# Performance work log

Measured on AMD Instinct MI355X. Metric: run time of the kernel, lower is better.

## Reference

```python
import jax, jax.numpy as jnp
import numpy as np

LEVELS = 16
FEATURES = 2
HASHMAP_SIZE = 524288  # 2**19
BASE_RES = 16
PER_LEVEL_SCALE = 1.5
N_POINTS = 2097152  # 2**21

# Per-level grid resolutions, computed exactly like the torch code: int(base*scale**l)
_RES = np.array([int(BASE_RES * PER_LEVEL_SCALE ** l) for l in range(LEVELS)], dtype=np.float32)

# Instant-NGP spatial hash primes
_P1, _P2, _P3 = np.int32(73856093), np.int32(19349663), np.int32(83492791)


def setup_inputs() -> dict:
    key = jax.random.key(0)
    k1, k2 = jax.random.split(key)
    x = jax.random.uniform(k1, (N_POINTS, 3), dtype=jnp.float32)
    # Stacked learned hash tables: [L, T, F], init randn*0.01 as in the module
    tables = jax.random.normal(k2, (LEVELS, HASHMAP_SIZE, FEATURES), dtype=jnp.float32) * 0.01
    return {"x": x, "tables": tables}


def reference(x, tables):
    # x: [N, 3] float; tables: [L, T, F] float
    res = jnp.asarray(_RES)                       # [L]
    pos = x[None, :, :] * res[:, None, None]      # [L, N, 3]
    p = jnp.floor(pos).astype(jnp.int32)          # [L, N, 3] (matches torch .int())
    # Spatial hash with int32 wrap-around, identical to torch int32 semantics
    h = (p[..., 0] * _P1) ^ (p[..., 1] * _P2) ^ (p[..., 2] * _P3)
    idx = jnp.mod(h, np.int32(HASHMAP_SIZE))      # [L, N], nonnegative (sign of divisor)
    emb = jax.vmap(lambda t, i: t[i])(tables, idx)  # [L, N, F] per-level gather
    n = x.shape[0]
    # concat over levels along last dim -> [N, L*F]
    return jnp.transpose(emb, (1, 0, 2)).reshape(n, LEVELS * FEATURES)
```

## Files before the change

### kernel.cpp

```cpp
#include <hip/hip_runtime.h>

#define LEVELS 16
#define TSIZE 524288
#define TMASK (TSIZE - 1)
#define TPB 256
#define GPPT 8
#define CHUNK (TPB * GPPT)

typedef float f2v __attribute__((ext_vector_type(2)));
typedef float f4v __attribute__((ext_vector_type(4)));

__device__ __constant__ float c_res[LEVELS] = {
    16.f, 24.f, 36.f, 54.f, 81.f, 121.f, 182.f, 273.f,
    410.f, 615.f, 922.f, 1383.f, 2075.f, 3113.f, 4670.f, 7006.f
};

__device__ __forceinline__ unsigned hash_idx(float px, float py, float pz, float r)
{
    const int ix = (int)floorf(px * r);
    const int iy = (int)floorf(py * r);
    const int iz = (int)floorf(pz * r);
    const unsigned h = (unsigned)ix * 73856093u
                     ^ (unsigned)iy * 19349663u
                     ^ (unsigned)iz * 83492791u;
    return h & TMASK;
}



__global__ __launch_bounds__(TPB) void hash_kernel(
    const float* __restrict__ x,
    unsigned* __restrict__ idxw,
    int n)
{
    __shared__ float xs[CHUNK * 3];
    const int c = blockIdx.x;
    const int t = threadIdx.x;
    const long long base = (long long)c * CHUNK;
    unsigned* __restrict__ islab = idxw + (size_t)c * LEVELS * CHUNK;

    if (base + CHUNK <= n) {
        const f4v* __restrict__ xg = reinterpret_cast<const f4v*>(x + 3 * base);
#pragma unroll
        for (int j = 0; j < 6; ++j) {
            const int s = j * TPB + t;
            *reinterpret_cast<f4v*>(&xs[4 * s]) = xg[s];
        }
        __syncthreads();

#pragma unroll
        for (int j = 0; j < GPPT; ++j) {
            const int local = j * TPB + t;
            const float px = xs[3 * local + 0];
            const float py = xs[3 * local + 1];
            const float pz = xs[3 * local + 2];
#pragma unroll
            for (int l = 0; l < LEVELS; ++l)
                islab[l * CHUNK + local] = hash_idx(px, py, pz, c_res[l]);
        }
    } else {
        for (int j = 0; j < GPPT; ++j) {
            const int local = j * TPB + t;
            const long long p = base + local;
            if (p < n) {
                const float px = x[3 * p + 0];
                const float py = x[3 * p + 1];
                const float pz = x[3 * p + 2];
                for (int l = 0; l < LEVELS; ++l)
                    islab[l * CHUNK + local] = hash_idx(px, py, pz, c_res[l]);
            }
        }
    }
}

__global__ __launch_bounds__(TPB) void gather_kernel(
    const unsigned* __restrict__ idxr,
    const float* __restrict__ tables,
    f2v* __restrict__ ws,
    int n, int bpl)
{
    const int b = blockIdx.x;
    const int half = b / (8 * bpl);
    const int r = b % (8 * bpl);
    const int level = half * 8 + (r & 7);
    const int c = r >> 3;
    const int t = threadIdx.x;

    const float* __restrict__ tbl = tables + (size_t)level * (TSIZE * 2);
    f2v* __restrict__ slab = ws + ((size_t)c * LEVELS + level) * CHUNK;
    const unsigned* __restrict__ islab = idxr + ((size_t)c * LEVELS + level) * CHUNK;
    const long long base = (long long)c * CHUNK;

    if (base + CHUNK <= n) {
        unsigned idx[GPPT];
#pragma unroll
        for (int j = 0; j < GPPT; ++j)
            idx[j] = islab[j * TPB + t];

        f2v e[GPPT];
#pragma unroll
        for (int j = 0; j < GPPT; ++j)
            e[j] = *reinterpret_cast<const f2v*>(tbl + 2 * (size_t)idx[j]);

#pragma unroll
        for (int j = 0; j < GPPT; ++j)
            __builtin_nontemporal_store(e[j], slab + j * TPB + t);
    } else {
        for (int j = 0; j < GPPT; ++j) {
            const int local = j * TPB + t;
            if (base + local < n) {
                const unsigned id = islab[local];
                const f2v e = *reinterpret_cast<const f2v*>(tbl + 2 * (size_t)id);
                __builtin_nontemporal_store(e, slab + local);
            }
        }
    }
}

__global__ __launch_bounds__(TPB) void gather_x_kernel(
    const float* __restrict__ x,
    const float* __restrict__ tables,
    f2v* __restrict__ ws,
    int n, int bpl)
{
    const int b = blockIdx.x;
    const int half = b / (8 * bpl);
    const int r = b % (8 * bpl);
    const int level = half * 8 + (r & 7);
    const int c = r >> 3;
    const int t = threadIdx.x;

    const float rs = c_res[level];
    const float* __restrict__ tbl = tables + (size_t)level * (TSIZE * 2);
    f2v* __restrict__ slab = ws + ((size_t)c * LEVELS + level) * CHUNK;
    const long long base = (long long)c * CHUNK;

    if (base + CHUNK <= n) {
        const float* __restrict__ xb = x + 3 * base;
        float px[GPPT], py[GPPT], pz[GPPT];
#pragma unroll
        for (int j = 0; j < GPPT; ++j) {
            const int local = j * TPB + t;
            px[j] = xb[3 * local + 0];
            py[j] = xb[3 * local + 1];
            pz[j] = xb[3 * local + 2];
        }
        unsigned idx[GPPT];
#pragma unroll
        for (int j = 0; j < GPPT; ++j)
            idx[j] = hash_idx(px[j], py[j], pz[j], rs);
        f2v e[GPPT];
#pragma unroll
        for (int j = 0; j < GPPT; ++j)
            e[j] = *reinterpret_cast<const f2v*>(tbl + 2 * (size_t)idx[j]);
#pragma unroll
        for (int j = 0; j < GPPT; ++j)
            __builtin_nontemporal_store(e[j], slab + j * TPB + t);
    } else {
#pragma unroll
        for (int j = 0; j < GPPT; ++j) {
            const int local = j * TPB + t;
            const long long p = base + local;
            if (p < n) {
                const float qx = x[3 * p + 0];
                const float qy = x[3 * p + 1];
                const float qz = x[3 * p + 2];
                const unsigned idx = hash_idx(qx, qy, qz, rs);
                const f2v e = *reinterpret_cast<const f2v*>(tbl + 2 * (size_t)idx);
                __builtin_nontemporal_store(e, slab + local);
            }
        }
    }
}

__global__ __launch_bounds__(TPB) void assemble_kernel(
    const f2v* __restrict__ ws,
    float* __restrict__ out,
    int n)
{
    const int c = blockIdx.x;
    const int t = threadIdx.x;
    const int q = t & 7;
    const int sub = t >> 3;

    const f2v* __restrict__ wa = ws + ((size_t)c * LEVELS + 2 * q) * CHUNK;
    const f2v* __restrict__ wb = wa + CHUNK;
    const long long base = (long long)c * CHUNK;

    if (base + CHUNK <= n) {
#pragma unroll 8
        for (int u = 0; u < CHUNK / 64; ++u) {
            const int lp = 2 * (u * 32 + sub);
            const f4v a = __builtin_nontemporal_load(
                reinterpret_cast<const f4v*>(wa + lp));
            const f4v b = __builtin_nontemporal_load(
                reinterpret_cast<const f4v*>(wb + lp));
            f4v v0, v1;
            v0.x = a.x; v0.y = a.y; v0.z = b.x; v0.w = b.y;
            v1.x = a.z; v1.y = a.w; v1.z = b.z; v1.w = b.w;
            float* row = out + (size_t)(base + lp) * (2 * LEVELS) + 4 * q;
            __builtin_nontemporal_store(v0, reinterpret_cast<f4v*>(row));
            __builtin_nontemporal_store(v1, reinterpret_cast<f4v*>(row + 2 * LEVELS));
        }
    } else {
#pragma unroll 8
        for (int u = 0; u < CHUNK / 32; ++u) {
            const int lp = u * 32 + sub;
            const long long pt = base + lp;
            if (pt < n) {
                const f2v a = __builtin_nontemporal_load(wa + lp);
                const f2v b = __builtin_nontemporal_load(wb + lp);
                f4v v;
                v.x = a.x; v.y = a.y; v.z = b.x; v.w = b.y;
                __builtin_nontemporal_store(
                    v, reinterpret_cast<f4v*>(out + (size_t)pt * (2 * LEVELS) + 4 * q));
            }
        }
    }
}

#define ROWW 34
__global__ __launch_bounds__(TPB) void hashgrid_fused(
    const float* __restrict__ x,
    const float* __restrict__ tables,
    float* __restrict__ out,
    int n)
{
    __shared__ float lds[TPB * ROWW];
    const int t = threadIdx.x;

    for (long long base = (long long)blockIdx.x * TPB; base < n;
         base += (long long)gridDim.x * TPB) {
        const int p = (int)base + t;
        float px = 0.f, py = 0.f, pz = 0.f;
        if (p < n) {
            px = x[3 * (size_t)p + 0];
            py = x[3 * (size_t)p + 1];
            pz = x[3 * (size_t)p + 2];
        }
#pragma unroll
        for (int l = 0; l < LEVELS; ++l) {
            if (p < n) {
                const unsigned idx = hash_idx(px, py, pz, c_res[l]);
                const f2v e = *reinterpret_cast<const f2v*>(
                    tables + (((size_t)l * TSIZE + idx) << 1));
                *reinterpret_cast<f2v*>(lds + t * ROWW + 2 * l) = e;
            }
            __syncthreads();
        }
#pragma unroll
        for (int it = 0; it < 8; ++it) {
            const int lp = it * 32 + (t >> 3);
            const int qq = t & 7;
            const int gp = (int)base + lp;
            if (gp < n) {
                const f2v a = *reinterpret_cast<const f2v*>(lds + lp * ROWW + 4 * qq);
                const f2v b = *reinterpret_cast<const f2v*>(lds + lp * ROWW + 4 * qq + 2);
                f4v v;
                v.x = a.x; v.y = a.y; v.z = b.x; v.w = b.y;
                __builtin_nontemporal_store(
                    v, reinterpret_cast<f4v*>(out + (size_t)gp * (2 * LEVELS) + 4 * qq));
            }
        }
        __syncthreads();
    }
}

extern "C" void kernel_launch(void* const* d_in, const int* in_sizes, int n_in,
                              void* d_out, int out_size, void* d_ws, size_t ws_size,
                              hipStream_t stream)
{
    const float* x      = (const float*)d_in[0];
    const float* tables = (const float*)d_in[1];
    float* out          = (float*)d_out;
    const int n = in_sizes[0] / 3;

    const int bpl = (n + CHUNK - 1) / CHUNK;
    const size_t slab_bytes = (size_t)bpl * LEVELS * CHUNK * sizeof(f2v);
    const size_t idx_bytes  = (size_t)bpl * LEVELS * CHUNK * sizeof(unsigned);

    if (ws_size < slab_bytes) {
        int grid = 1024;
        const int nblocks = (n + TPB - 1) / TPB;
        if (nblocks < grid) grid = nblocks;
        hashgrid_fused<<<grid, TPB, 0, stream>>>(x, tables, out, n);
        return;
    }

    f2v* ws = (f2v*)d_ws;

    if (ws_size >= slab_bytes + idx_bytes) {
        unsigned* idxw = (unsigned*)((char*)d_ws + slab_bytes);
        hash_kernel<<<bpl, TPB, 0, stream>>>(x, idxw, n);
        gather_kernel<<<2 * 8 * bpl, TPB, 0, stream>>>(idxw, tables, ws, n, bpl);
    } else {
        gather_x_kernel<<<2 * 8 * bpl, TPB, 0, stream>>>(x, tables, ws, n, bpl);
    }
    assemble_kernel<<<bpl, TPB, 0, stream>>>(ws, out, n);
}
```

Measured before the change: 321.5 us.

## Fold coarse-level gathers into hash kernel and remap gather block scheduling

The hash kernel now gathers the embeddings for the two coarsest levels itself and writes them straight into the workspace slabs. This removes the index write and re-read for those levels, and the small tables fit in cache. The gather kernel now covers only levels 2-15, using a new block-to-work mapping that splits the level×chunk range into eight contiguous segments interleaved across block IDs. The risk is that the hash kernel gets longer from its added gather latency, and the new mapping changes which tables are in cache together.

```diff
diff --git a/kernel.cpp b/kernel.cpp
--- a/kernel.cpp
+++ b/kernel.cpp
@@ -15,22 +15,25 @@
     410.f, 615.f, 922.f, 1383.f, 2075.f, 3113.f, 4670.f, 7006.f
 };
 
+__device__ __forceinline__ unsigned hash_iii(int ix, int iy, int iz)
+{
+    return ((unsigned)ix * 73856093u
+          ^ (unsigned)iy * 19349663u
+          ^ (unsigned)iz * 83492791u) & TMASK;
+}
+
 __device__ __forceinline__ unsigned hash_idx(float px, float py, float pz, float r)
 {
-    const int ix = (int)floorf(px * r);
-    const int iy = (int)floorf(py * r);
-    const int iz = (int)floorf(pz * r);
-    const unsigned h = (unsigned)ix * 73856093u
-                     ^ (unsigned)iy * 19349663u
-                     ^ (unsigned)iz * 83492791u;
-    return h & TMASK;
+    return hash_iii((int)floorf(px * r), (int)floorf(py * r), (int)floorf(pz * r));
 }
 
 
 
 __global__ __launch_bounds__(TPB) void hash_kernel(
     const float* __restrict__ x,
+    const float* __restrict__ tables,
     unsigned* __restrict__ idxw,
+    f2v* __restrict__ ws,
     int n)
 {
     __shared__ float xs[CHUNK * 3];
@@ -38,6 +41,10 @@
     const int t = threadIdx.x;
     const long long base = (long long)c * CHUNK;
     unsigned* __restrict__ islab = idxw + (size_t)c * LEVELS * CHUNK;
+    f2v* __restrict__ slab0 = ws + (size_t)c * LEVELS * CHUNK;
+    f2v* __restrict__ slab1 = slab0 + CHUNK;
+    const float* __restrict__ t0 = tables;
+    const float* __restrict__ t1 = tables + (size_t)TSIZE * 2;
 
     if (base + CHUNK <= n) {
         const f4v* __restrict__ xg = reinterpret_cast<const f4v*>(x + 3 * base);
@@ -54,9 +61,18 @@
             const float px = xs[3 * local + 0];
             const float py = xs[3 * local + 1];
             const float pz = xs[3 * local + 2];
-#pragma unroll
-            for (int l = 0; l < LEVELS; ++l)
+
+            const unsigned id0 = hash_idx(px, py, pz, 16.f);
+            const unsigned id1 = hash_idx(px, py, pz, 24.f);
+            const f2v e0 = *reinterpret_cast<const f2v*>(t0 + 2 * (size_t)id0);
+            const f2v e1 = *reinterpret_cast<const f2v*>(t1 + 2 * (size_t)id1);
+
+#pragma unroll
+            for (int l = 2; l < LEVELS; ++l)
                 islab[l * CHUNK + local] = hash_idx(px, py, pz, c_res[l]);
+
+            __builtin_nontemporal_store(e0, slab0 + local);
+            __builtin_nontemporal_store(e1, slab1 + local);
         }
     } else {
         for (int j = 0; j < GPPT; ++j) {
@@ -66,7 +82,11 @@
                 const float px = x[3 * p + 0];
                 const float py = x[3 * p + 1];
                 const float pz = x[3 * p + 2];
-                for (int l = 0; l < LEVELS; ++l)
+                const unsigned id0 = hash_idx(px, py, pz, 16.f);
+                const unsigned id1 = hash_idx(px, py, pz, 24.f);
+                slab0[local] = *reinterpret_cast<const f2v*>(t0 + 2 * (size_t)id0);
+                slab1[local] = *reinterpret_cast<const f2v*>(t1 + 2 * (size_t)id1);
+                for (int l = 2; l < LEVELS; ++l)
                     islab[l * CHUNK + local] = hash_idx(px, py, pz, c_res[l]);
             }
         }
@@ -77,13 +97,16 @@
     const unsigned* __restrict__ idxr,
     const float* __restrict__ tables,
     f2v* __restrict__ ws,
-    int n, int bpl)
-{
-    const int b = blockIdx.x;
-    const int half = b / (8 * bpl);
-    const int r = b % (8 * bpl);
-    const int level = half * 8 + (r & 7);
-    const int c = r >> 3;
+    int n, int bpl, int lvl_start, int nlv)
+{
+    const long long total = (long long)nlv * bpl;
+    const int k = blockIdx.x & 7;
+    const long long s = blockIdx.x >> 3;
+    const long long w = ((total * k) >> 3) + s;
+    if (w >= ((total * (k + 1)) >> 3)) return;
+    const int lrel = (int)(w / bpl);
+    const int level = lvl_start + lrel;
+    const int c = (int)(w - (long long)lrel * bpl);
     const int t = threadIdx.x;
 
     const float* __restrict__ tbl = tables + (size_t)level * (TSIZE * 2);
@@ -291,8 +314,10 @@
 
     if (ws_size >= slab_bytes + idx_bytes) {
         unsigned* idxw = (unsigned*)((char*)d_ws + slab_bytes);
-        hash_kernel<<<bpl, TPB, 0, stream>>>(x, idxw, n);
-        gather_kernel<<<2 * 8 * bpl, TPB, 0, stream>>>(idxw, tables, ws, n, bpl);
+        const long long total_hi = 14LL * bpl;
+        hash_kernel<<<bpl, TPB, 0, stream>>>(x, tables, idxw, ws, n);
+        gather_kernel<<<(int)(8 * ((total_hi + 7) / 8)), TPB, 0, stream>>>(
+            idxw, tables, ws, n, bpl, 2, 14);
     } else {
         gather_x_kernel<<<2 * 8 * bpl, TPB, 0, stream>>>(x, tables, ws, n, bpl);
     }
```

After: 311.8 us. 1.03x faster.
